# Performance work log

Measured on AMD Instinct MI355X. Metric: run time of the kernel, lower is better.

Reference implementation:

```python
import jax, jax.numpy as jnp
import numpy as np

B, N, D, D1, R, O = 256, 32, 128, 128, 8, 8


def setup_inputs() -> dict:
    key = jax.random.key(0)
    k = jax.random.split(key, 7)
    return {
        "center_h": jax.random.normal(k[0], (B, D), dtype=jnp.float32),
        "raw_neighbors": jax.random.normal(k[1], (B, N, D), dtype=jnp.float32),
        "M": jax.random.normal(k[2], (R, O, D, D1), dtype=jnp.float32) * 0.05,
        "b": jax.random.normal(k[3], (R, O, D1), dtype=jnp.float32) * 0.01,
        "center_o": jax.random.randint(k[4], (B,), 0, O, dtype=jnp.int32),
        "s_types": jax.random.randint(k[5], (B, N), 0, R, dtype=jnp.int32),
        "o_types": jax.random.randint(k[6], (B, N), 0, O, dtype=jnp.int32),
    }


def reference(center_h, raw_neighbors, M, b, center_o, s_types, o_types):
    # --- center projection: for each example b, all relations r, with o = center_o[b]
    M_center = M[:, center_o]                      # [R, B, D, D1]
    b_center = b[:, center_o]                      # [R, B, D1]
    h_center = jnp.einsum('bd,rbdj->brj', center_h, M_center)  # [B, R, D1]
    h_center = h_center + jnp.transpose(b_center, (1, 0, 2))

    # --- neighbor projection: per-(example, neighbor) (s_type, o_type)-indexed matrix
    s_idx = jnp.maximum(s_types, 0)
    o_idx = jnp.maximum(o_types, 0)
    M_neighbor = M[s_idx, o_idx]                   # [B, N, D, D1] (large gather)
    h_neighbor = jnp.einsum('bnd,bndj->bnj', raw_neighbors, M_neighbor)  # [B, N, D1]
    h_neighbor = h_neighbor + b[s_idx, o_idx]

    # tf.nn.gelu default is exact (erf-based)
    return (jax.nn.gelu(h_center, approximate=False),
            jax.nn.gelu(h_neighbor, approximate=False))
```

## Files before the change

kernel.cpp:

```cpp
#include <hip/hip_runtime.h>
#include <math.h>

#define NPAIR 64
#define NCENTER 2048
#define WCAP 48
#define RSLOT 32

typedef __attribute__((ext_vector_type(8))) short bfrag8;
typedef __attribute__((ext_vector_type(8))) unsigned short u16x8;
typedef __attribute__((ext_vector_type(4))) float f32x4;

__device__ __forceinline__ float gelu_f(float v) {
    return 0.5f * v * (1.0f + erff(v * 0.70710678118654752f));
}
__device__ __forceinline__ unsigned short f2bf(float f) {
    unsigned int u = __float_as_uint(f);
    return (unsigned short)((u + 0x7FFFu + ((u >> 16) & 1u)) >> 16);
}

__global__ __launch_bounds__(256, 4) void fused_kernel(
    const float* __restrict__ center_h,
    const float* __restrict__ raw_neighbors,
    const float* __restrict__ Mg,
    const float* __restrict__ bias,
    const int* __restrict__ center_o,
    const int* __restrict__ s_types,
    const int* __restrict__ o_types,
    float* __restrict__ out)
{
    __shared__ __align__(16) unsigned short Mbt[64 * 128];
    __shared__ __align__(16) unsigned short Xs[RSLOT * 128];
    __shared__ int list[4 * WCAP];
    __shared__ int cnts[4];
    __shared__ int rowid[RSLOT];

    const int t    = threadIdx.x;
    const int wave = t >> 6, lane = t & 63;
    const int pair = blockIdx.x & 63;
    const int rest = blockIdx.x >> 6;
    const int ch   = rest & 1;
    const int slice = rest >> 1;
    const int r0 = pair >> 3, o0 = pair & 7;

    const int4 svv = ((const int4*)s_types)[slice * 256 + t];
    const int4 ovv = ((const int4*)o_types)[slice * 256 + t];
    const int my_b  = slice * 32 + wave * 8 + (lane & 7);
    const int my_co = center_o[my_b];

    const int lane16 = t & 15, dblk = t >> 4;
    float g[4][8];
    {
        const float* mp = Mg + pair * 16384 + (dblk * 8) * 128 + ch * 64;
        #pragma unroll
        for (int i = 0; i < 4; ++i)
            #pragma unroll
            for (int r = 0; r < 8; ++r)
                g[i][r] = mp[r * 128 + 16 * i + lane16];
    }

    int cw = 0;
    {
        const bool match = (lane < 8) && (my_co == o0);
        const unsigned long long mk = __ballot(match);
        const int pre = __builtin_amdgcn_mbcnt_hi(
            (unsigned)(mk >> 32), __builtin_amdgcn_mbcnt_lo((unsigned)mk, 0));
        if (match) {
            const int pos = cw + pre;
            if (pos < WCAP) list[wave * WCAP + pos] = my_b * 8 + r0;
        }
        cw += __popcll(mk);
    }
    {
        const int ss[4] = { svv.x, svv.y, svv.z, svv.w };
        const int oo[4] = { ovv.x, ovv.y, ovv.z, ovv.w };
        const int base_nid = slice * 1024 + t * 4;
        #pragma unroll
        for (int j = 0; j < 4; ++j) {
            const int s = ss[j] < 0 ? 0 : ss[j];
            const int o = oo[j] < 0 ? 0 : oo[j];
            const bool match = (s == r0) & (o == o0);
            const unsigned long long mk = __ballot(match);
            const int pre = __builtin_amdgcn_mbcnt_hi(
                (unsigned)(mk >> 32), __builtin_amdgcn_mbcnt_lo((unsigned)mk, 0));
            if (match) {
                const int pos = cw + pre;
                if (pos < WCAP) list[wave * WCAP + pos] = NCENTER + base_nid + j;
            }
            cw += __popcll(mk);
            if (cw > WCAP) cw = WCAP;
        }
    }
    if (lane == 0) cnts[wave] = cw;

    #pragma unroll
    for (int i = 0; i < 4; ++i) {
        const int c = 16 * i + lane16;
        u16x8 w;
        #pragma unroll
        for (int r = 0; r < 8; ++r) w[r] = f2bf(g[i][r]);
        *(u16x8*)((char*)Mbt + c * 256 + ((dblk ^ lane16) << 4)) = w;
    }
    __syncthreads();

    const int c0_ = cnts[0], c1_ = cnts[1], c2_ = cnts[2];
    const int cnt = c0_ + c1_ + c2_ + cnts[3];

    const int lo16 = lane & 15, hi4 = lane >> 4;
    const int c_loc = wave * 16 + lo16;
    const int colg  = ch * 64 + c_loc;
    const float bv = bias[pair * 128 + colg];

    for (int base = 0; base < cnt; base += RSLOT) {
        const int csz = (cnt - base < RSLOT) ? (cnt - base) : RSLOT;

        if (t < RSLOT) {
            int id = -1;
            int a = base + t;
            if (a < cnt) {
                int sw = 0;
                if (a >= c0_) { a -= c0_; sw = 1;
                    if (a >= c1_) { a -= c1_; sw = 2;
                        if (a >= c2_) { a -= c2_; sw = 3; } } }
                id = list[sw * WCAP + a];
            }
            rowid[t] = id;
        }
        __syncthreads();

        #pragma unroll
        for (int i = 0; i < 2; ++i) {
            const int flat = i * 256 + t;
            const int slot = flat >> 4, chg = flat & 15;
            const int id = rowid[slot];
            u16x8 w = {0, 0, 0, 0, 0, 0, 0, 0};
            if (id >= 0) {
                const float* xp = (id < NCENTER) ? center_h + (id >> 3) * 128
                                                 : raw_neighbors + (id - NCENTER) * 128;
                const float4 x0 = *(const float4*)(xp + chg * 8);
                const float4 x1 = *(const float4*)(xp + chg * 8 + 4);
                w[0] = f2bf(x0.x); w[1] = f2bf(x0.y); w[2] = f2bf(x0.z); w[3] = f2bf(x0.w);
                w[4] = f2bf(x1.x); w[5] = f2bf(x1.y); w[6] = f2bf(x1.z); w[7] = f2bf(x1.w);
            }
            *(u16x8*)((char*)Xs + slot * 256 + ((chg ^ (slot & 15)) << 4)) = w;
        }
        __syncthreads();

        f32x4 accA = {bv, bv, bv, bv};
        f32x4 accC = accA;
        #pragma unroll
        for (int k = 0; k < 4; ++k) {
            const int dch = 4 * k + hi4;
            const int gsl = (dch ^ lo16) << 4;
            const bfrag8 aA = *(const bfrag8*)((const char*)Xs  + lo16 * 256 + gsl);
            const bfrag8 aB = *(const bfrag8*)((const char*)Xs  + (16 + lo16) * 256 + gsl);
            const bfrag8 b0 = *(const bfrag8*)((const char*)Mbt + c_loc * 256 + gsl);
            accA = __builtin_amdgcn_mfma_f32_16x16x32_bf16(aA, b0, accA, 0, 0, 0);
            accC = __builtin_amdgcn_mfma_f32_16x16x32_bf16(aB, b0, accC, 0, 0, 0);
        }

        #pragma unroll
        for (int j = 0; j < 4; ++j) {
            const int sA = hi4 * 4 + j;
            if (sA < csz) out[rowid[sA] * 128 + colg] = gelu_f(accA[j]);
            const int sB = 16 + hi4 * 4 + j;
            if (sB < csz) out[rowid[sB] * 128 + colg] = gelu_f(accC[j]);
        }
        __syncthreads();
    }
}

extern "C" void kernel_launch(void* const* d_in, const int* in_sizes, int n_in,
                              void* d_out, int out_size, void* d_ws, size_t ws_size,
                              hipStream_t stream) {
    const float* center_h      = (const float*)d_in[0];
    const float* raw_neighbors = (const float*)d_in[1];
    const float* M             = (const float*)d_in[2];
    const float* bias          = (const float*)d_in[3];
    const int*   center_o      = (const int*)d_in[4];
    const int*   s_types       = (const int*)d_in[5];
    const int*   o_types       = (const int*)d_in[6];
    float* out = (float*)d_out;

    fused_kernel<<<dim3(NPAIR * 16), dim3(256), 0, stream>>>(
        center_h, raw_neighbors, M, bias, center_o, s_types, o_types, out);
}
```

Before: 11.91 us.

## Load MFMA A-fragments directly from global memory, drop X staging in LDS

Each wave now resolves its own row ids and loads activation rows from global memory straight into MFMA A-fragment registers, converting to bf16 in registers. This removes the shared Xs and rowid buffers and the three block-wide barriers per row chunk. In exchange, each of the four waves reloads the same activation rows, so global/L2 traffic for X rises fourfold. List lookups are also recomputed per output element.

New measurement: 16.08 us. +35.0%, slower.

```diff
diff --git a/kernel.cpp b/kernel.cpp
--- a/kernel.cpp
+++ b/kernel.cpp
@@ -29,10 +29,8 @@
     float* __restrict__ out)
 {
     __shared__ __align__(16) unsigned short Mbt[64 * 128];
-    __shared__ __align__(16) unsigned short Xs[RSLOT * 128];
     __shared__ int list[4 * WCAP];
     __shared__ int cnts[4];
-    __shared__ int rowid[RSLOT];
 
     const int t    = threadIdx.x;
     const int wave = t >> 6, lane = t & 63;
@@ -111,61 +109,77 @@
     const float bv = bias[pair * 128 + colg];
 
     for (int base = 0; base < cnt; base += RSLOT) {
-        const int csz = (cnt - base < RSLOT) ? (cnt - base) : RSLOT;
-
-        if (t < RSLOT) {
-            int id = -1;
-            int a = base + t;
-            if (a < cnt) {
-                int sw = 0;
-                if (a >= c0_) { a -= c0_; sw = 1;
-                    if (a >= c1_) { a -= c1_; sw = 2;
-                        if (a >= c2_) { a -= c2_; sw = 3; } } }
-                id = list[sw * WCAP + a];
-            }
-            rowid[t] = id;
-        }
-        __syncthreads();
-
-        #pragma unroll
-        for (int i = 0; i < 2; ++i) {
-            const int flat = i * 256 + t;
-            const int slot = flat >> 4, chg = flat & 15;
-            const int id = rowid[slot];
-            u16x8 w = {0, 0, 0, 0, 0, 0, 0, 0};
-            if (id >= 0) {
-                const float* xp = (id < NCENTER) ? center_h + (id >> 3) * 128
-                                                 : raw_neighbors + (id - NCENTER) * 128;
-                const float4 x0 = *(const float4*)(xp + chg * 8);
-                const float4 x1 = *(const float4*)(xp + chg * 8 + 4);
-                w[0] = f2bf(x0.x); w[1] = f2bf(x0.y); w[2] = f2bf(x0.z); w[3] = f2bf(x0.w);
-                w[4] = f2bf(x1.x); w[5] = f2bf(x1.y); w[6] = f2bf(x1.z); w[7] = f2bf(x1.w);
-            }
-            *(u16x8*)((char*)Xs + slot * 256 + ((chg ^ (slot & 15)) << 4)) = w;
-        }
-        __syncthreads();
+        int idA = 0, idB = 0;
+        {
+            int p = base + lo16;
+            if (p < cnt) {
+                int a = p, sw = 0;
+                if (a >= c0_) { a -= c0_; sw = 1;
+                    if (a >= c1_) { a -= c1_; sw = 2;
+                        if (a >= c2_) { a -= c2_; sw = 3; } } }
+                idA = list[sw * WCAP + a];
+            }
+            p = base + 16 + lo16;
+            if (p < cnt) {
+                int a = p, sw = 0;
+                if (a >= c0_) { a -= c0_; sw = 1;
+                    if (a >= c1_) { a -= c1_; sw = 2;
+                        if (a >= c2_) { a -= c2_; sw = 3; } } }
+                idB = list[sw * WCAP + a];
+            }
+        }
+        const float* xA = (idA < NCENTER) ? center_h + (idA >> 3) * 128
+                                          : raw_neighbors + (idA - NCENTER) * 128;
+        const float* xB = (idB < NCENTER) ? center_h + (idB >> 3) * 128
+                                          : raw_neighbors + (idB - NCENTER) * 128;
+
+        float4 fa[4][2], fb[4][2];
+        #pragma unroll
+        for (int k = 0; k < 4; ++k) {
+            const int off = k * 32 + hi4 * 8;
+            fa[k][0] = *(const float4*)(xA + off);
+            fa[k][1] = *(const float4*)(xA + off + 4);
+            fb[k][0] = *(const float4*)(xB + off);
+            fb[k][1] = *(const float4*)(xB + off + 4);
+        }
 
         f32x4 accA = {bv, bv, bv, bv};
         f32x4 accC = accA;
         #pragma unroll
         for (int k = 0; k < 4; ++k) {
+            bfrag8 aA, aB;
+            #pragma unroll
+            for (int e = 0; e < 4; ++e) {
+                aA[e]     = (short)f2bf(((const float*)&fa[k][0])[e]);
+                aA[e + 4] = (short)f2bf(((const float*)&fa[k][1])[e]);
+                aB[e]     = (short)f2bf(((const float*)&fb[k][0])[e]);
+                aB[e + 4] = (short)f2bf(((const float*)&fb[k][1])[e]);
+            }
             const int dch = 4 * k + hi4;
-            const int gsl = (dch ^ lo16) << 4;
-            const bfrag8 aA = *(const bfrag8*)((const char*)Xs  + lo16 * 256 + gsl);
-            const bfrag8 aB = *(const bfrag8*)((const char*)Xs  + (16 + lo16) * 256 + gsl);
-            const bfrag8 b0 = *(const bfrag8*)((const char*)Mbt + c_loc * 256 + gsl);
+            const bfrag8 b0 = *(const bfrag8*)((const char*)Mbt + c_loc * 256 + ((dch ^ lo16) << 4));
             accA = __builtin_amdgcn_mfma_f32_16x16x32_bf16(aA, b0, accA, 0, 0, 0);
             accC = __builtin_amdgcn_mfma_f32_16x16x32_bf16(aB, b0, accC, 0, 0, 0);
         }
 
         #pragma unroll
         for (int j = 0; j < 4; ++j) {
-            const int sA = hi4 * 4 + j;
-            if (sA < csz) out[rowid[sA] * 128 + colg] = gelu_f(accA[j]);
-            const int sB = 16 + hi4 * 4 + j;
-            if (sB < csz) out[rowid[sB] * 128 + colg] = gelu_f(accC[j]);
-        }
-        __syncthreads();
+            int p = base + hi4 * 4 + j;
+            if (p < cnt) {
+                int a = p, sw = 0;
+                if (a >= c0_) { a -= c0_; sw = 1;
+                    if (a >= c1_) { a -= c1_; sw = 2;
+                        if (a >= c2_) { a -= c2_; sw = 3; } } }
+                out[list[sw * WCAP + a] * 128 + colg] = gelu_f(accA[j]);
+            }
+            p = base + 16 + hi4 * 4 + j;
+            if (p < cnt) {
+                int a = p, sw = 0;
+                if (a >= c0_) { a -= c0_; sw = 1;
+                    if (a >= c1_) { a -= c1_; sw = 2;
+                        if (a >= c2_) { a -= c2_; sw = 3; } } }
+                out[list[sw * WCAP + a] * 128 + colg] = gelu_f(accC[j]);
+            }
+        }
     }
 }
 
```
